# Kernel optimization log

Hardware: AMD Instinct MI355X
Metric: run time of the kernel (lower is better)

The kernel has to match this reference:

```python
import jax, jax.numpy as jnp
import numpy as np

EPS = 1e-6

def layer_norm(x, g, b):
    mu = jnp.mean(x, axis=-1, keepdims=True)
    var = jnp.mean((x - mu) ** 2, axis=-1, keepdims=True)
    return g * (x - mu) / jnp.sqrt(var + EPS) + b

def linear_mha(v_in, k_in, q_in, wq, bq, wk, bk, wv, bv, wo, bo, num_heads, d_model):
    b, s, _ = q_in.shape
    dv = d_model // num_heads
    q = q_in @ wq + bq                       # [b, s, h] (depth-1 per head)
    k = k_in @ wk + bk                       # [b, s, h]
    v = (v_in @ wv + bv).reshape(b, s, num_heads, dv).transpose(0, 2, 1, 3)  # [b,h,s,dv]
    q = q.transpose(0, 2, 1)                 # [b, h, s]
    k = k.transpose(0, 2, 1)                 # [b, h, s]
    # phi(k)^T v collapses seq: rank-1 per head -> [b, h, dv]
    kv = jnp.einsum('bhs,bhsd->bhd', jax.nn.sigmoid(k), v)
    # NOTE: tf.cumsum(axis=1) on shape (b, h, 1, dv) cumsums over the HEAD axis
    s_cum = jnp.cumsum(kv, axis=1)           # [b, h, dv]
    out = jnp.einsum('bhs,bhd->bhsd', jax.nn.sigmoid(q), s_cum)  # [b,h,s,dv]
    out = out.transpose(0, 2, 1, 3).reshape(b, s, d_model)
    return out @ wo + bo

def setup_inputs() -> dict:
    key = jax.random.key(0)
    ks = jax.random.split(key, 24)
    B, S, D, H, F = 4, 4096, 1024, 16, 4096
    gl = lambda k, shp: jax.random.uniform(k, shp, jnp.float32,
        -jnp.sqrt(6.0 / (shp[0] + shp[1])), jnp.sqrt(6.0 / (shp[0] + shp[1])))
    inp = {
        'x': jax.random.normal(ks[0], (B, S, D), jnp.float32),
        'enc': jax.random.normal(ks[1], (B, S, D), jnp.float32),
        'wq1': gl(ks[2], (D, H)), 'bq1': jnp.zeros((H,), jnp.float32),
        'wk1': gl(ks[3], (D, H)), 'bk1': jnp.zeros((H,), jnp.float32),
        'wv1': gl(ks[4], (D, D)), 'bv1': jnp.zeros((D,), jnp.float32),
        'wo1': gl(ks[5], (D, D)), 'bo1': jnp.zeros((D,), jnp.float32),
        'wq2': gl(ks[6], (D, H)), 'bq2': jnp.zeros((H,), jnp.float32),
        'wk2': gl(ks[7], (D, H)), 'bk2': jnp.zeros((H,), jnp.float32),
        'wv2': gl(ks[8], (D, D)), 'bv2': jnp.zeros((D,), jnp.float32),
        'wo2': gl(ks[9], (D, D)), 'bo2': jnp.zeros((D,), jnp.float32),
        'wf1': gl(ks[10], (D, F)), 'bf1': jnp.zeros((F,), jnp.float32),
        'wf2': gl(ks[11], (F, D)), 'bf2': jnp.zeros((D,), jnp.float32),
        'g1': jnp.ones((D,), jnp.float32), 'be1': jnp.zeros((D,), jnp.float32),
        'g2': jnp.ones((D,), jnp.float32), 'be2': jnp.zeros((D,), jnp.float32),
        'g3': jnp.ones((D,), jnp.float32), 'be3': jnp.zeros((D,), jnp.float32),
    }
    return inp

def reference(x, enc, wq1, bq1, wk1, bk1, wv1, bv1, wo1, bo1,
              wq2, bq2, wk2, bk2, wv2, bv2, wo2, bo2,
              wf1, bf1, wf2, bf2, g1, be1, g2, be2, g3, be3):
    H, D = 16, x.shape[-1]
    attn1 = linear_mha(x, x, x, wq1, bq1, wk1, bk1, wv1, bv1, wo1, bo1, H, D)
    out1 = layer_norm(attn1 + x, g1, be1)
    attn2 = linear_mha(enc, enc, out1, wq2, bq2, wk2, bk2, wv2, bv2, wo2, bo2, H, D)
    out2 = layer_norm(attn2 + out1, g2, be2)
    ffn = jax.nn.relu(out2 @ wf1 + bf1) @ wf2 + bf2
    out3 = layer_norm(ffn + out2, g3, be3)
    return (out3, jnp.zeros_like(out3), jnp.zeros_like(out3))
```

## Files before the change

kernel.cpp:

```cpp
#include <hip/hip_runtime.h>
#include <cstdint>

typedef unsigned short u16;
typedef __bf16 bf16x8 __attribute__((ext_vector_type(8)));
typedef float f32x4 __attribute__((ext_vector_type(4)));

__device__ __forceinline__ float bf2f(u16 h) {
  union { uint32_t u; float f; } v; v.u = (uint32_t)h << 16; return v.f;
}
__device__ __forceinline__ u16 f2bf(float f) {
  union { float f; uint32_t u; } v; v.f = f;
  uint32_t r = v.u + 0x7fffu + ((v.u >> 16) & 1u);
  return (u16)(r >> 16);
}
__device__ __forceinline__ float sigmoidf_(float x) {
  return 1.0f / (1.0f + __expf(-x));
}
__device__ __forceinline__ void load_lds16(const void* g, void* l) {
  __builtin_amdgcn_global_load_lds(
      (const __attribute__((address_space(1))) void*)g,
      (__attribute__((address_space(3))) void*)l, 16, 0, 0);
}
#define BAR() __builtin_amdgcn_s_barrier()

__global__ __launch_bounds__(256) void cvt_f2b(const float* __restrict__ in,
                                               u16* __restrict__ out) {
  long i = ((long)blockIdx.x * 256 + threadIdx.x) * 4;
  float4 v = *(const float4*)(in + i);
  uint2 o;
  o.x = (uint32_t)f2bf(v.x) | ((uint32_t)f2bf(v.y) << 16);
  o.y = (uint32_t)f2bf(v.z) | ((uint32_t)f2bf(v.w) << 16);
  *((uint2*)(out + i)) = o;
}

__global__ __launch_bounds__(256) void transpose_cvt(
    const float* __restrict__ in, u16* __restrict__ out, int K, int N) {
  __shared__ float t[32][33];
  int n0 = blockIdx.x * 32, k0 = blockIdx.y * 32;
  int tx = threadIdx.x & 31, ty = threadIdx.x >> 5;
#pragma unroll
  for (int i = 0; i < 32; i += 8)
    t[ty + i][tx] = in[(long)(k0 + ty + i) * N + n0 + tx];
  __syncthreads();
#pragma unroll
  for (int i = 0; i < 32; i += 8)
    out[(long)(n0 + ty + i) * K + k0 + tx] = f2bf(t[tx][ty + i]);
}

__global__ __launch_bounds__(256) void proj_mfma(
    const u16* __restrict__ xq, const u16* __restrict__ xk,
    const float* __restrict__ wq, const float* __restrict__ bq,
    const float* __restrict__ wk, const float* __restrict__ bk,
    float* __restrict__ qout, float* __restrict__ kout) {
  __shared__ __attribute__((aligned(16))) u16 wt[2][16384];
  __shared__ __attribute__((aligned(16))) float red[4][64][8];
  const int tid = threadIdx.x;
  for (int kq = 0; kq < 4; kq++) {
    int k = kq * 256 + tid;
    const float4* q4 = (const float4*)(wq + (long)k * 16);
    const float4* k4 = (const float4*)(wk + (long)k * 16);
#pragma unroll
    for (int p = 0; p < 4; p++) {
      float4 qv = q4[p], kv = k4[p];
      float qf[4] = {qv.x, qv.y, qv.z, qv.w};
      float kf[4] = {kv.x, kv.y, kv.z, kv.w};
#pragma unroll
      for (int j = 0; j < 4; j++) {
        int c = p * 4 + j;
        int off = (c * 2048 + k * 2) ^ ((c & 7) << 4);
        *(u16*)((char*)wt[0] + off) = f2bf(qf[j]);
        *(u16*)((char*)wt[1] + off) = f2bf(kf[j]);
      }
    }
  }
  __syncthreads();
  const int wv = tid >> 6, lane = tid & 63;
  const int lrow = lane & 15, g = lane >> 4;
  const long tok0 = (long)blockIdx.x * 16;
  const u16* xqp = xq + (tok0 + lrow) * 1024 + wv * 256 + g * 8;
  const u16* xkp = xk + (tok0 + lrow) * 1024 + wv * 256 + g * 8;
  const int swz = (lrow & 7) << 4;
  const int wbase = lrow * 2048 + wv * 512 + g * 16;
  f32x4 accq = {}, acck = {};
#pragma unroll
  for (int mf = 0; mf < 8; mf++) {
    bf16x8 aq_ = *(const bf16x8*)(xqp + mf * 32);
    bf16x8 ak_ = *(const bf16x8*)(xkp + mf * 32);
    int off = (wbase + mf * 64) ^ swz;
    bf16x8 bq_ = *(const bf16x8*)((const char*)wt[0] + off);
    bf16x8 bk_ = *(const bf16x8*)((const char*)wt[1] + off);
    accq = __builtin_amdgcn_mfma_f32_16x16x32_bf16(aq_, bq_, accq, 0, 0, 0);
    acck = __builtin_amdgcn_mfma_f32_16x16x32_bf16(ak_, bk_, acck, 0, 0, 0);
  }
  *(f32x4*)&red[wv][lane][0] = accq;
  *(f32x4*)&red[wv][lane][4] = acck;
  __syncthreads();
  if (tid < 64) {
    f32x4 q0 = *(const f32x4*)&red[0][tid][0];
    f32x4 k0 = *(const f32x4*)&red[0][tid][4];
#pragma unroll
    for (int w = 1; w < 4; w++) {
      q0 += *(const f32x4*)&red[w][tid][0];
      k0 += *(const f32x4*)&red[w][tid][4];
    }
    int col = tid & 15, r0 = (tid >> 4) * 4;
    float bqv = bq[col], bkv = bk[col];
#pragma unroll
    for (int i = 0; i < 4; i++) {
      qout[(tok0 + r0 + i) * 16 + col] = q0[i] + bqv;
      kout[(tok0 + r0 + i) * 16 + col] = k0[i] + bkv;
    }
  }
}

__global__ __launch_bounds__(256) void ksum(const float* __restrict__ kp,
                                            const u16* __restrict__ xb,
                                            float* __restrict__ ypart,
                                            float* __restrict__ spart) {
  __shared__ float sk[256][17];
  const int tid = threadIdx.x;
  const int cc = blockIdx.x, sc = blockIdx.y, b = blockIdx.z;
  const int cl = tid & 63, sg = tid >> 6;
  const int col = cc * 64 + cl;
  float acc[16];
#pragma unroll
  for (int h = 0; h < 16; h++) acc[h] = 0.f;
  float ss = 0.f;
  for (int tile = 0; tile < 4; tile++) {
    const int s0 = sc * 1024 + tile * 256;
    const float* kr = kp + ((long)b * 4096 + s0 + tid) * 16;
#pragma unroll
    for (int p = 0; p < 4; p++) {
      float4 kv4 = *(const float4*)(kr + p * 4);
      sk[tid][p * 4 + 0] = sigmoidf_(kv4.x);
      sk[tid][p * 4 + 1] = sigmoidf_(kv4.y);
      sk[tid][p * 4 + 2] = sigmoidf_(kv4.z);
      sk[tid][p * 4 + 3] = sigmoidf_(kv4.w);
    }
    __syncthreads();
    if (tid < 16) {
      float s_ = 0.f;
      for (int i = 0; i < 256; i++) s_ += sk[i][tid];
      ss += s_;
    }
    const u16* xr = xb + ((long)b * 4096 + s0 + sg * 64) * 1024 + col;
    for (int j = 0; j < 64; j++) {
      float xv = bf2f(xr[(long)j * 1024]);
      const float* skr = sk[sg * 64 + j];
#pragma unroll
      for (int h = 0; h < 16; h++) acc[h] += skr[h] * xv;
    }
    __syncthreads();
  }
  long pbase = (long)(b * 16 + sc * 4 + sg) * 16384 + col;
#pragma unroll
  for (int h = 0; h < 16; h++) ypart[pbase + h * 1024] = acc[h];
  if (tid < 16) spart[(b * 4 + sc) * 16 + tid] = ss;
}

__global__ __launch_bounds__(64) void kv_small(const float* __restrict__ ypart,
                                               const float* __restrict__ spart,
                                               const float* __restrict__ wv,
                                               const float* __restrict__ bv,
                                               float* __restrict__ kv) {
  __shared__ float yl[1024];
  const int b = blockIdx.x >> 4, h = blockIdx.x & 15, d = threadIdx.x;
  for (int c = d; c < 1024; c += 64) {
    float s_ = 0.f;
    const float* yp = ypart + (long)b * 16 * 16384 + h * 1024 + c;
#pragma unroll
    for (int p = 0; p < 16; p++) s_ += yp[(long)p * 16384];
    yl[c] = s_;
  }
  __syncthreads();
  float ss = 0.f;
#pragma unroll
  for (int s_ = 0; s_ < 4; s_++) ss += spart[(b * 4 + s_) * 16 + h];
  float acc = 0.f;
  const float* wcol = wv + h * 64 + d;
  for (int c = 0; c < 1024; c++) acc += yl[c] * wcol[(long)c * 1024];
  kv[(b * 16 + h) * 64 + d] = acc + ss * bv[h * 64 + d];
}

__global__ __launch_bounds__(64) void kv_cumsum(const float* __restrict__ kv,
                                                float* __restrict__ scum) {
  int b = blockIdx.x, d = threadIdx.x;
  float run = 0.f;
  for (int h = 0; h < 16; h++) {
    run += kv[(b * 16 + h) * 64 + d];
    scum[(b * 16 + h) * 64 + d] = run;
  }
}

__global__ __launch_bounds__(256) void zker(const float* __restrict__ scum,
                                            const float* __restrict__ wo,
                                            float* __restrict__ z) {
  __shared__ float sc_[64];
  const int tid = threadIdx.x;
  const int b = blockIdx.x >> 4, h = blockIdx.x & 15;
  if (tid < 64) sc_[tid] = scum[(b * 16 + h) * 64 + tid];
  __syncthreads();
  float4 acc = make_float4(0.f, 0.f, 0.f, 0.f);
  for (int d = 0; d < 64; d++) {
    float s_ = sc_[d];
    float4 w = ((const float4*)(wo + (long)(h * 64 + d) * 1024))[tid];
    acc.x += s_ * w.x; acc.y += s_ * w.y;
    acc.z += s_ * w.z; acc.w += s_ * w.w;
  }
  ((float4*)(z + (long)(b * 16 + h) * 1024))[tid] = acc;
}

template <int OMODE>
__global__ __launch_bounds__(256) void ln_attn(
    const float* __restrict__ qp, const float* __restrict__ z,
    const float* __restrict__ bo, const float* __restrict__ r,
    const float* __restrict__ g, const float* __restrict__ be,
    float* __restrict__ outf, u16* __restrict__ outb) {
  __shared__ float zs[16][1024];
  __shared__ float sq16[16];
  __shared__ float s1[4], s2[4];
  const int tid = threadIdx.x;
  const int b = blockIdx.x >> 8;
  const float4* zg = (const float4*)(z + (long)b * 16384);
  float4* zl = (float4*)zs;
#pragma unroll
  for (int i = 0; i < 16; i++) zl[i * 256 + tid] = zg[i * 256 + tid];
  float4 gv = ((const float4*)g)[tid];
  float4 bev = ((const float4*)be)[tid];
  float4 bov = ((const float4*)bo)[tid];
  const int wid = tid >> 6, lane = tid & 63;
  for (int rr_ = 0; rr_ < 16; rr_++) {
    long row = (long)blockIdx.x * 16 + rr_;
    if (tid < 16) sq16[tid] = sigmoidf_(qp[row * 16 + tid]);
    __syncthreads();
    float4 rv = ((const float4*)(r + row * 1024))[tid];
    float y0 = bov.x + rv.x, y1 = bov.y + rv.y;
    float y2 = bov.z + rv.z, y3 = bov.w + rv.w;
#pragma unroll
    for (int h = 0; h < 16; h++) {
      float s_ = sq16[h];
      float4 zv = *(const float4*)&zs[h][tid * 4];
      y0 += s_ * zv.x; y1 += s_ * zv.y; y2 += s_ * zv.z; y3 += s_ * zv.w;
    }
    float s = y0 + y1 + y2 + y3;
    float q = y0 * y0 + y1 * y1 + y2 * y2 + y3 * y3;
#pragma unroll
    for (int o = 32; o > 0; o >>= 1) {
      s += __shfl_down(s, o);
      q += __shfl_down(q, o);
    }
    if (lane == 0) { s1[wid] = s; s2[wid] = q; }
    __syncthreads();
    s = s1[0] + s1[1] + s1[2] + s1[3];
    q = s2[0] + s2[1] + s2[2] + s2[3];
    float mu = s * (1.f / 1024.f);
    float var = q * (1.f / 1024.f) - mu * mu;
    float inv = rsqrtf(fmaxf(var, 0.f) + 1e-6f);
    float o0 = gv.x * (y0 - mu) * inv + bev.x;
    float o1 = gv.y * (y1 - mu) * inv + bev.y;
    float o2 = gv.z * (y2 - mu) * inv + bev.z;
    float o3 = gv.w * (y3 - mu) * inv + bev.w;
    ((float4*)(outf + row * 1024))[tid] = make_float4(o0, o1, o2, o3);
    if (OMODE == 2) {
      uint2 ob;
      ob.x = (uint32_t)f2bf(o0) | ((uint32_t)f2bf(o1) << 16);
      ob.y = (uint32_t)f2bf(o2) | ((uint32_t)f2bf(o3) << 16);
      ((uint2*)(outb + row * 1024))[tid] = ob;
    }
    __syncthreads();
  }
}

template <int ACT>
__global__ __launch_bounds__(512) void gemm256(
    const u16* __restrict__ A, const u16* __restrict__ BT,
    const float* __restrict__ bias, u16* __restrict__ C, int M, int N,
    int K) {
  __shared__ __attribute__((aligned(16))) u16 lds[65536];
  const int tid = threadIdx.x;
  const int wid = tid >> 6, lane = tid & 63;
  const int wm = wid >> 2, wn = wid & 3;
  const int lrow = lane & 15, g = lane >> 4;

  int nwg = gridDim.x * gridDim.y;
  int orig = blockIdx.y * gridDim.x + blockIdx.x;
  int wg = (nwg & 7) ? orig : ((orig & 7) * (nwg >> 3) + (orig >> 3));
  const long bn = (long)(wg % gridDim.x) * 256;
  const long bm = (long)(wg / gridDim.x) * 256;

  const int rr = wid * 16 + (lane >> 2);
  const int esrc = ((lane & 3) * 8) ^ (((lane >> 5) & 1) * 16);
  const u16* Abase = A + (bm + rr) * (long)K + esrc;
  const u16* Bbase = BT + (bn + rr) * (long)K + esrc;
  const long jstep = (long)128 * K;
  char* ldsc = (char*)lds;
  const int ldsw = wid * 1024;

  const int swr = ((lrow >> 3) & 1) * 32;
  const int aoff = (wm * 128 + lrow) * 64 + ((g * 16) ^ swr);
  const int boff = 32768 + (wn * 64 + lrow) * 64 + ((g * 16) ^ swr);

  f32x4 acc[8][4] = {};
  const int KT = K >> 6;

  auto stage2 = [&](int buf, int kk, int kt, int half) {
    int dA = buf * 65536 + kk * 16384 + ldsw;
    if (half == 0) {
      const u16* sA = Abase + (long)kt * 64 + kk * 32;
      load_lds16(sA, ldsc + dA);
      load_lds16(sA + jstep, ldsc + dA + 8192);
    } else {
      const u16* sB = Bbase + (long)kt * 64 + kk * 32;
      load_lds16(sB, ldsc + dA + 32768);
      load_lds16(sB + jstep, ldsc + dA + 40960);
    }
  };

#define LDAB8(BUF, KK)                                                      \
  {                                                                         \
    const char* _b = ldsc + (BUF) * 65536 + (KK) * 16384;                   \
    _Pragma("unroll") for (int m = 0; m < 4; m++)                           \
        af[m] = *(const bf16x8*)(_b + aoff + m * 1024);                     \
    _Pragma("unroll") for (int n = 0; n < 4; n++)                           \
        bq[n] = *(const bf16x8*)(_b + boff + n * 1024);                     \
  }
#define LDA4(BUF, KK)                                                       \
  {                                                                         \
    const char* _b = ldsc + (BUF) * 65536 + (KK) * 16384;                   \
    _Pragma("unroll") for (int m = 4; m < 8; m++)                           \
        af[m] = *(const bf16x8*)(_b + aoff + m * 1024);                     \
  }
#define MMA16(M0)                                                           \
  __builtin_amdgcn_s_setprio(1);                                            \
  _Pragma("unroll") for (int m = M0; m < M0 + 4; m++)                       \
  _Pragma("unroll") for (int n = 0; n < 4; n++)                             \
      acc[m][n] = __builtin_amdgcn_mfma_f32_16x16x32_bf16(af[m], bq[n],     \
                                                          acc[m][n], 0, 0,  \
                                                          0);               \
  __builtin_amdgcn_s_setprio(0);
#define WLG0() asm volatile("s_waitcnt lgkmcnt(0)" ::: "memory")
#define WVM4() asm volatile("s_waitcnt vmcnt(4)" ::: "memory")
#define WVM0() asm volatile("s_waitcnt vmcnt(0)" ::: "memory")

  bf16x8 af[8], bq[4];

  stage2(0, 0, 0, 0);
  stage2(0, 0, 0, 1);
  stage2(0, 1, 0, 0);
  stage2(0, 1, 0, 1);
  WVM4();
  BAR();

  for (int kt = 0; kt + 1 < KT; ++kt) {
    const int b0 = kt & 1, b1 = b0 ^ 1;
    LDAB8(b0, 0);
    stage2(b1, 0, kt + 1, 0);
    BAR(); WLG0();
    MMA16(0);
    BAR();
    LDA4(b0, 0);
    stage2(b1, 0, kt + 1, 1);
    WVM4();
    BAR(); WLG0();
    MMA16(4);
    BAR();
    LDAB8(b0, 1);
    stage2(b1, 1, kt + 1, 0);
    BAR(); WLG0();
    MMA16(0);
    BAR();
    LDA4(b0, 1);
    stage2(b1, 1, kt + 1, 1);
    WVM4();
    BAR(); WLG0();
    MMA16(4);
    BAR();
  }
  {
    const int b0 = (KT - 1) & 1;
    LDAB8(b0, 0);
    BAR(); WLG0();
    MMA16(0);
    BAR();
    LDA4(b0, 0);
    WVM0();
    BAR(); WLG0();
    MMA16(4);
    BAR();
    LDAB8(b0, 1);
    BAR(); WLG0();
    MMA16(0);
    BAR();
    LDA4(b0, 1);
    BAR(); WLG0();
    MMA16(4);
    BAR();
  }

#pragma unroll
  for (int n = 0; n < 4; n++) {
    int cl = wn * 64 + n * 16 + lrow;
    float bb = bias[bn + cl];
#pragma unroll
    for (int m = 0; m < 8; m++) {
      int rl = wm * 128 + m * 16 + g * 4;
#pragma unroll
      for (int i = 0; i < 4; i++) {
        float v = acc[m][n][i] + bb;
        if (ACT == 1) v = fmaxf(v, 0.f);
        lds[(rl + i) * 256 + cl] = f2bf(v);
      }
    }
  }
  BAR();
  const uint4* lv = (const uint4*)lds;
#pragma unroll
  for (int it = 0; it < 16; it++) {
    int idx = it * 512 + tid;
    int row = idx >> 5;
    int cu = (idx & 31) * 8;
    *(uint4*)&C[(bm + row) * (long)N + bn + cu] = lv[idx];
  }
#undef LDAB8
#undef LDA4
#undef MMA16
#undef WLG0
#undef WVM4
#undef WVM0
}

__global__ __launch_bounds__(256) void ln_res(const u16* __restrict__ a,
                                              const float* __restrict__ r,
                                              const float* __restrict__ g,
                                              const float* __restrict__ be,
                                              float* __restrict__ outf) {
  long row = blockIdx.x;
  int tid = threadIdx.x;
  uint2 av = ((const uint2*)(a + row * 1024))[tid];
  float4 rv = ((const float4*)(r + row * 1024))[tid];
  float y[4];
  y[0] = bf2f((u16)(av.x & 0xffff)) + rv.x;
  y[1] = bf2f((u16)(av.x >> 16)) + rv.y;
  y[2] = bf2f((u16)(av.y & 0xffff)) + rv.z;
  y[3] = bf2f((u16)(av.y >> 16)) + rv.w;
  float s = y[0] + y[1] + y[2] + y[3];
  float q = y[0] * y[0] + y[1] * y[1] + y[2] * y[2] + y[3] * y[3];
#pragma unroll
  for (int o = 32; o > 0; o >>= 1) {
    s += __shfl_down(s, o);
    q += __shfl_down(q, o);
  }
  __shared__ float s1[4], s2[4];
  int wid = tid >> 6, lane = tid & 63;
  if (lane == 0) { s1[wid] = s; s2[wid] = q; }
  __syncthreads();
  s = s1[0] + s1[1] + s1[2] + s1[3];
  q = s2[0] + s2[1] + s2[2] + s2[3];
  float mu = s * (1.f / 1024.f);
  float var = q * (1.f / 1024.f) - mu * mu;
  float inv = rsqrtf(fmaxf(var, 0.f) + 1e-6f);
  float4 gv = ((const float4*)g)[tid], bv = ((const float4*)be)[tid];
  float o0 = gv.x * (y[0] - mu) * inv + bv.x;
  float o1 = gv.y * (y[1] - mu) * inv + bv.y;
  float o2 = gv.z * (y[2] - mu) * inv + bv.z;
  float o3 = gv.w * (y[3] - mu) * inv + bv.w;
  ((float4*)(outf + row * 1024))[tid] = make_float4(o0, o1, o2, o3);
}

extern "C" void kernel_launch(void* const* d_in, const int* in_sizes, int n_in,
                              void* d_out, int out_size, void* d_ws,
                              size_t ws_size, hipStream_t stream) {
  const float* x   = (const float*)d_in[0];
  const float* enc = (const float*)d_in[1];
  const float* wq1 = (const float*)d_in[2];  const float* bq1 = (const float*)d_in[3];
  const float* wk1 = (const float*)d_in[4];  const float* bk1 = (const float*)d_in[5];
  const float* wv1 = (const float*)d_in[6];  const float* bv1 = (const float*)d_in[7];
  const float* wo1 = (const float*)d_in[8];  const float* bo1 = (const float*)d_in[9];
  const float* wq2 = (const float*)d_in[10]; const float* bq2 = (const float*)d_in[11];
  const float* wk2 = (const float*)d_in[12]; const float* bk2 = (const float*)d_in[13];
  const float* wv2 = (const float*)d_in[14]; const float* bv2 = (const float*)d_in[15];
  const float* wo2 = (const float*)d_in[16]; const float* bo2 = (const float*)d_in[17];
  const float* wf1 = (const float*)d_in[18]; const float* bf1 = (const float*)d_in[19];
  const float* wf2 = (const float*)d_in[20]; const float* bf2 = (const float*)d_in[21];
  const float* g1 = (const float*)d_in[22];  const float* be1 = (const float*)d_in[23];
  const float* g2 = (const float*)d_in[24];  const float* be2 = (const float*)d_in[25];
  const float* g3 = (const float*)d_in[26];  const float* be3 = (const float*)d_in[27];
  (void)in_sizes; (void)n_in; (void)out_size; (void)ws_size;

  const size_t S = (size_t)16384 * 1024;
  float* O0 = (float*)d_out;

  char* base = (char*)d_ws;
  size_t off = 0;
  auto alloc = [&](size_t bytes) -> void* {
    void* p = base + off;
    off += (bytes + 255) & ~(size_t)255;
    return p;
  };
  u16* WT1    = (u16*)alloc((size_t)4096 * 1024 * 2);
  u16* WT2    = (u16*)alloc((size_t)4096 * 1024 * 2);
  float* qb   = (float*)alloc((size_t)16384 * 16 * 4);
  float* kb   = (float*)alloc((size_t)16384 * 16 * 4);
  float* ypart= (float*)alloc((size_t)4 * 16 * 16 * 1024 * 4);
  float* spart= (float*)alloc((size_t)4 * 4 * 16 * 4);
  float* kvb  = (float*)alloc((size_t)4 * 16 * 64 * 4);
  float* scm  = (float*)alloc((size_t)4 * 16 * 64 * 4);
  float* zb   = (float*)alloc((size_t)4 * 16 * 1024 * 4);
  u16* FA     = (u16*)alloc(S * 2);
  u16* XB     = (u16*)alloc(S * 2);
  u16* FM     = (u16*)alloc((size_t)16384 * 4096 * 2);
  u16* O1b    = (u16*)alloc(S * 2);
  u16* O2b    = (u16*)alloc(S * 2);
  float* O1f  = (float*)alloc(S * 4);
  float* O2f  = (float*)alloc(S * 4);

  const int T = 16384;
  dim3 blk(256), gblk(512);

  cvt_f2b<<<16384, blk, 0, stream>>>(x, XB);
  proj_mfma<<<1024, blk, 0, stream>>>(XB, XB, wq1, bq1, wk1, bk1, qb, kb);
  ksum<<<dim3(16, 4, 4), blk, 0, stream>>>(kb, XB, ypart, spart);
  kv_small<<<64, 64, 0, stream>>>(ypart, spart, wv1, bv1, kvb);
  kv_cumsum<<<4, 64, 0, stream>>>(kvb, scm);
  zker<<<64, blk, 0, stream>>>(scm, wo1, zb);
  ln_attn<2><<<1024, blk, 0, stream>>>(qb, zb, bo1, x, g1, be1, O1f, O1b);

  cvt_f2b<<<16384, blk, 0, stream>>>(enc, XB);
  proj_mfma<<<1024, blk, 0, stream>>>(O1b, XB, wq2, bq2, wk2, bk2, qb, kb);
  ksum<<<dim3(16, 4, 4), blk, 0, stream>>>(kb, XB, ypart, spart);
  kv_small<<<64, 64, 0, stream>>>(ypart, spart, wv2, bv2, kvb);
  kv_cumsum<<<4, 64, 0, stream>>>(kvb, scm);
  zker<<<64, blk, 0, stream>>>(scm, wo2, zb);
  ln_attn<2><<<1024, blk, 0, stream>>>(qb, zb, bo2, O1f, g2, be2, O2f, O2b);

  transpose_cvt<<<dim3(128, 32), blk, 0, stream>>>(wf1, WT1, 1024, 4096);
  transpose_cvt<<<dim3(32, 128), blk, 0, stream>>>(wf2, WT2, 4096, 1024);
  gemm256<1><<<dim3(16, 64), gblk, 0, stream>>>(O2b, WT1, bf1, FM, T, 4096, 1024);
  gemm256<0><<<dim3(4, 64), gblk, 0, stream>>>(FM, WT2, bf2, FA, T, 1024, 4096);
  ln_res<<<16384, blk, 0, stream>>>(FA, O2f, g3, be3, O0);

  hipMemsetAsync((float*)d_out + S, 0, 2 * S * 4, stream);
}
```

Baseline: 697.3 us.

## Fuse fp32-to-bf16 conversion into projection, widen ksum tiles, fold cumsum into zker

Removes the separate cvt_f2b passes over x and enc. proj_mfma now converts fp32 activations to bf16 in registers, and ksum reads fp32 directly. ksum now gives each thread two columns and splits the sequence into eight chunks instead of four, and its sigmoid column sum is now a two-level parallel reduction. kv_small now uses 256 threads with a split reduction, and the kv_cumsum kernel is folded into zker as a per-block prefix loop. The aim is to cut bf16 round-trip traffic and launch count, at the cost of reading fp32 inputs twice in ksum and a larger partials buffer.

```diff
diff --git a/kernel.cpp b/kernel.cpp
--- a/kernel.cpp
+++ b/kernel.cpp
@@ -21,17 +21,14 @@
       (const __attribute__((address_space(1))) void*)g,
       (__attribute__((address_space(3))) void*)l, 16, 0, 0);
 }
+__device__ __forceinline__ bf16x8 cvt8(const float* p) {
+  float4 a = *(const float4*)p, b = *(const float4*)(p + 4);
+  union { u16 u[8]; bf16x8 v; } r;
+  r.u[0] = f2bf(a.x); r.u[1] = f2bf(a.y); r.u[2] = f2bf(a.z); r.u[3] = f2bf(a.w);
+  r.u[4] = f2bf(b.x); r.u[5] = f2bf(b.y); r.u[6] = f2bf(b.z); r.u[7] = f2bf(b.w);
+  return r.v;
+}
 #define BAR() __builtin_amdgcn_s_barrier()
-
-__global__ __launch_bounds__(256) void cvt_f2b(const float* __restrict__ in,
-                                               u16* __restrict__ out) {
-  long i = ((long)blockIdx.x * 256 + threadIdx.x) * 4;
-  float4 v = *(const float4*)(in + i);
-  uint2 o;
-  o.x = (uint32_t)f2bf(v.x) | ((uint32_t)f2bf(v.y) << 16);
-  o.y = (uint32_t)f2bf(v.z) | ((uint32_t)f2bf(v.w) << 16);
-  *((uint2*)(out + i)) = o;
-}
 
 __global__ __launch_bounds__(256) void transpose_cvt(
     const float* __restrict__ in, u16* __restrict__ out, int K, int N) {
@@ -47,8 +44,9 @@
     out[(long)(n0 + ty + i) * K + k0 + tx] = f2bf(t[tx][ty + i]);
 }
 
+template <int QBF>
 __global__ __launch_bounds__(256) void proj_mfma(
-    const u16* __restrict__ xq, const u16* __restrict__ xk,
+    const void* __restrict__ xq_, const float* __restrict__ xk,
     const float* __restrict__ wq, const float* __restrict__ bq,
     const float* __restrict__ wk, const float* __restrict__ bk,
     float* __restrict__ qout, float* __restrict__ kout) {
@@ -77,15 +75,18 @@
   const int wv = tid >> 6, lane = tid & 63;
   const int lrow = lane & 15, g = lane >> 4;
   const long tok0 = (long)blockIdx.x * 16;
-  const u16* xqp = xq + (tok0 + lrow) * 1024 + wv * 256 + g * 8;
-  const u16* xkp = xk + (tok0 + lrow) * 1024 + wv * 256 + g * 8;
+  const long arow = (tok0 + lrow) * 1024 + wv * 256 + g * 8;
   const int swz = (lrow & 7) << 4;
   const int wbase = lrow * 2048 + wv * 512 + g * 16;
   f32x4 accq = {}, acck = {};
 #pragma unroll
   for (int mf = 0; mf < 8; mf++) {
-    bf16x8 aq_ = *(const bf16x8*)(xqp + mf * 32);
-    bf16x8 ak_ = *(const bf16x8*)(xkp + mf * 32);
+    bf16x8 aq_;
+    if (QBF)
+      aq_ = *(const bf16x8*)((const u16*)xq_ + arow + mf * 32);
+    else
+      aq_ = cvt8((const float*)xq_ + arow + mf * 32);
+    bf16x8 ak_ = cvt8(xk + arow + mf * 32);
     int off = (wbase + mf * 64) ^ swz;
     bf16x8 bq_ = *(const bf16x8*)((const char*)wt[0] + off);
     bf16x8 bk_ = *(const bf16x8*)((const char*)wt[1] + off);
@@ -114,91 +115,111 @@
 }
 
 __global__ __launch_bounds__(256) void ksum(const float* __restrict__ kp,
-                                            const u16* __restrict__ xb,
+                                            const float* __restrict__ x,
                                             float* __restrict__ ypart,
                                             float* __restrict__ spart) {
-  __shared__ float sk[256][17];
+  __shared__ __attribute__((aligned(16))) float sk[256][20];
+  __shared__ float ssl[16][17];
   const int tid = threadIdx.x;
   const int cc = blockIdx.x, sc = blockIdx.y, b = blockIdx.z;
   const int cl = tid & 63, sg = tid >> 6;
-  const int col = cc * 64 + cl;
-  float acc[16];
-#pragma unroll
-  for (int h = 0; h < 16; h++) acc[h] = 0.f;
+  const int col0 = cc * 128 + cl;
+  float acc0[16], acc1[16];
+#pragma unroll
+  for (int h = 0; h < 16; h++) { acc0[h] = 0.f; acc1[h] = 0.f; }
   float ss = 0.f;
-  for (int tile = 0; tile < 4; tile++) {
-    const int s0 = sc * 1024 + tile * 256;
+  for (int tile = 0; tile < 2; tile++) {
+    const int s0 = sc * 512 + tile * 256;
     const float* kr = kp + ((long)b * 4096 + s0 + tid) * 16;
 #pragma unroll
     for (int p = 0; p < 4; p++) {
-      float4 kv4 = *(const float4*)(kr + p * 4);
-      sk[tid][p * 4 + 0] = sigmoidf_(kv4.x);
-      sk[tid][p * 4 + 1] = sigmoidf_(kv4.y);
-      sk[tid][p * 4 + 2] = sigmoidf_(kv4.z);
-      sk[tid][p * 4 + 3] = sigmoidf_(kv4.w);
+      float4 k4 = *(const float4*)(kr + p * 4);
+      *(float4*)&sk[tid][p * 4] = make_float4(
+          sigmoidf_(k4.x), sigmoidf_(k4.y), sigmoidf_(k4.z), sigmoidf_(k4.w));
+    }
+    __syncthreads();
+    {
+      int g2 = tid >> 4, h2 = tid & 15;
+      float s_ = 0.f;
+#pragma unroll
+      for (int i = 0; i < 16; i++) s_ += sk[g2 * 16 + i][h2];
+      ssl[g2][h2] = s_;
     }
     __syncthreads();
     if (tid < 16) {
       float s_ = 0.f;
-      for (int i = 0; i < 256; i++) s_ += sk[i][tid];
+#pragma unroll
+      for (int gg = 0; gg < 16; gg++) s_ += ssl[gg][tid];
       ss += s_;
     }
-    const u16* xr = xb + ((long)b * 4096 + s0 + sg * 64) * 1024 + col;
+    const float* xr = x + ((long)b * 4096 + s0 + sg * 64) * 1024 + col0;
     for (int j = 0; j < 64; j++) {
-      float xv = bf2f(xr[(long)j * 1024]);
-      const float* skr = sk[sg * 64 + j];
-#pragma unroll
-      for (int h = 0; h < 16; h++) acc[h] += skr[h] * xv;
+      float xv0 = xr[(long)j * 1024];
+      float xv1 = xr[(long)j * 1024 + 64];
+      const float4* skr = (const float4*)sk[sg * 64 + j];
+#pragma unroll
+      for (int p = 0; p < 4; p++) {
+        float4 s4 = skr[p];
+        acc0[p * 4 + 0] += s4.x * xv0; acc1[p * 4 + 0] += s4.x * xv1;
+        acc0[p * 4 + 1] += s4.y * xv0; acc1[p * 4 + 1] += s4.y * xv1;
+        acc0[p * 4 + 2] += s4.z * xv0; acc1[p * 4 + 2] += s4.z * xv1;
+        acc0[p * 4 + 3] += s4.w * xv0; acc1[p * 4 + 3] += s4.w * xv1;
+      }
     }
     __syncthreads();
   }
-  long pbase = (long)(b * 16 + sc * 4 + sg) * 16384 + col;
-#pragma unroll
-  for (int h = 0; h < 16; h++) ypart[pbase + h * 1024] = acc[h];
-  if (tid < 16) spart[(b * 4 + sc) * 16 + tid] = ss;
-}
-
-__global__ __launch_bounds__(64) void kv_small(const float* __restrict__ ypart,
-                                               const float* __restrict__ spart,
-                                               const float* __restrict__ wv,
-                                               const float* __restrict__ bv,
-                                               float* __restrict__ kv) {
+  long pbase = (long)(b * 32 + sc * 4 + sg) * 16384 + col0;
+#pragma unroll
+  for (int h = 0; h < 16; h++) {
+    ypart[pbase + h * 1024] = acc0[h];
+    ypart[pbase + h * 1024 + 64] = acc1[h];
+  }
+  if (tid < 16) spart[(b * 8 + sc) * 16 + tid] = ss;
+}
+
+__global__ __launch_bounds__(256) void kv_small(
+    const float* __restrict__ ypart, const float* __restrict__ spart,
+    const float* __restrict__ wvw, const float* __restrict__ bv,
+    float* __restrict__ kv) {
   __shared__ float yl[1024];
-  const int b = blockIdx.x >> 4, h = blockIdx.x & 15, d = threadIdx.x;
-  for (int c = d; c < 1024; c += 64) {
+  __shared__ float red[4][64];
+  const int tid = threadIdx.x;
+  const int b = blockIdx.x >> 4, h = blockIdx.x & 15;
+  for (int c = tid; c < 1024; c += 256) {
     float s_ = 0.f;
-    const float* yp = ypart + (long)b * 16 * 16384 + h * 1024 + c;
-#pragma unroll
-    for (int p = 0; p < 16; p++) s_ += yp[(long)p * 16384];
+    const float* yp = ypart + (long)(b * 32) * 16384 + h * 1024 + c;
+#pragma unroll
+    for (int p = 0; p < 32; p++) s_ += yp[(long)p * 16384];
     yl[c] = s_;
   }
   __syncthreads();
-  float ss = 0.f;
-#pragma unroll
-  for (int s_ = 0; s_ < 4; s_++) ss += spart[(b * 4 + s_) * 16 + h];
+  const int wv_ = tid >> 6, d = tid & 63;
   float acc = 0.f;
-  const float* wcol = wv + h * 64 + d;
-  for (int c = 0; c < 1024; c++) acc += yl[c] * wcol[(long)c * 1024];
-  kv[(b * 16 + h) * 64 + d] = acc + ss * bv[h * 64 + d];
-}
-
-__global__ __launch_bounds__(64) void kv_cumsum(const float* __restrict__ kv,
-                                                float* __restrict__ scum) {
-  int b = blockIdx.x, d = threadIdx.x;
-  float run = 0.f;
-  for (int h = 0; h < 16; h++) {
-    run += kv[(b * 16 + h) * 64 + d];
-    scum[(b * 16 + h) * 64 + d] = run;
-  }
-}
-
-__global__ __launch_bounds__(256) void zker(const float* __restrict__ scum,
+  const float* wcol = wvw + h * 64 + d;
+  for (int c = wv_ * 256; c < wv_ * 256 + 256; c++)
+    acc += yl[c] * wcol[(long)c * 1024];
+  red[wv_][d] = acc;
+  __syncthreads();
+  if (tid < 64) {
+    float ss = 0.f;
+#pragma unroll
+    for (int s_ = 0; s_ < 8; s_++) ss += spart[(b * 8 + s_) * 16 + h];
+    kv[(b * 16 + h) * 64 + tid] = red[0][tid] + red[1][tid] + red[2][tid] +
+                                  red[3][tid] + ss * bv[h * 64 + tid];
+  }
+}
+
+__global__ __launch_bounds__(256) void zker(const float* __restrict__ kvb,
                                             const float* __restrict__ wo,
                                             float* __restrict__ z) {
   __shared__ float sc_[64];
   const int tid = threadIdx.x;
   const int b = blockIdx.x >> 4, h = blockIdx.x & 15;
-  if (tid < 64) sc_[tid] = scum[(b * 16 + h) * 64 + tid];
+  if (tid < 64) {
+    float run = 0.f;
+    for (int hh = 0; hh <= h; hh++) run += kvb[(b * 16 + hh) * 64 + tid];
+    sc_[tid] = run;
+  }
   __syncthreads();
   float4 acc = make_float4(0.f, 0.f, 0.f, 0.f);
   for (int d = 0; d < 64; d++) {
@@ -501,13 +522,11 @@
   u16* WT2    = (u16*)alloc((size_t)4096 * 1024 * 2);
   float* qb   = (float*)alloc((size_t)16384 * 16 * 4);
   float* kb   = (float*)alloc((size_t)16384 * 16 * 4);
-  float* ypart= (float*)alloc((size_t)4 * 16 * 16 * 1024 * 4);
-  float* spart= (float*)alloc((size_t)4 * 4 * 16 * 4);
+  float* ypart= (float*)alloc((size_t)4 * 32 * 16 * 1024 * 4);
+  float* spart= (float*)alloc((size_t)4 * 8 * 16 * 4);
   float* kvb  = (float*)alloc((size_t)4 * 16 * 64 * 4);
-  float* scm  = (float*)alloc((size_t)4 * 16 * 64 * 4);
   float* zb   = (float*)alloc((size_t)4 * 16 * 1024 * 4);
   u16* FA     = (u16*)alloc(S * 2);
-  u16* XB     = (u16*)alloc(S * 2);
   u16* FM     = (u16*)alloc((size_t)16384 * 4096 * 2);
   u16* O1b    = (u16*)alloc(S * 2);
   u16* O2b    = (u16*)alloc(S * 2);
@@ -517,20 +536,16 @@
   const int T = 16384;
   dim3 blk(256), gblk(512);
 
-  cvt_f2b<<<16384, blk, 0, stream>>>(x, XB);
-  proj_mfma<<<1024, blk, 0, stream>>>(XB, XB, wq1, bq1, wk1, bk1, qb, kb);
-  ksum<<<dim3(16, 4, 4), blk, 0, stream>>>(kb, XB, ypart, spart);
-  kv_small<<<64, 64, 0, stream>>>(ypart, spart, wv1, bv1, kvb);
-  kv_cumsum<<<4, 64, 0, stream>>>(kvb, scm);
-  zker<<<64, blk, 0, stream>>>(scm, wo1, zb);
+  proj_mfma<0><<<1024, blk, 0, stream>>>(x, x, wq1, bq1, wk1, bk1, qb, kb);
+  ksum<<<dim3(8, 8, 4), blk, 0, stream>>>(kb, x, ypart, spart);
+  kv_small<<<64, blk, 0, stream>>>(ypart, spart, wv1, bv1, kvb);
+  zker<<<64, blk, 0, stream>>>(kvb, wo1, zb);
   ln_attn<2><<<1024, blk, 0, stream>>>(qb, zb, bo1, x, g1, be1, O1f, O1b);
 
-  cvt_f2b<<<16384, blk, 0, stream>>>(enc, XB);
-  proj_mfma<<<1024, blk, 0, stream>>>(O1b, XB, wq2, bq2, wk2, bk2, qb, kb);
-  ksum<<<dim3(16, 4, 4), blk, 0, stream>>>(kb, XB, ypart, spart);
-  kv_small<<<64, 64, 0, stream>>>(ypart, spart, wv2, bv2, kvb);
-  kv_cumsum<<<4, 64, 0, stream>>>(kvb, scm);
-  zker<<<64, blk, 0, stream>>>(scm, wo2, zb);
+  proj_mfma<1><<<1024, blk, 0, stream>>>(O1b, enc, wq2, bq2, wk2, bk2, qb, kb);
+  ksum<<<dim3(8, 8, 4), blk, 0, stream>>>(kb, enc, ypart, spart);
+  kv_small<<<64, blk, 0, stream>>>(ypart, spart, wv2, bv2, kvb);
+  zker<<<64, blk, 0, stream>>>(kvb, wo2, zb);
   ln_attn<2><<<1024, blk, 0, stream>>>(qb, zb, bo2, O1f, g2, be2, O2f, O2b);
 
   transpose_cvt<<<dim3(128, 32), blk, 0, stream>>>(wf1, WT1, 1024, 4096);
```

Measured after the change: 593.2 us. 1.18x faster.
